# Optimization experiments

Measured on AMD Instinct MI355X. Metric: run time of the kernel, lower is better.

The kernel has to match this reference:

```python
import jax, jax.numpy as jnp
import numpy as np

N_NODES = 50000
N_EDGES = 800000
IN_C, HID_C, OUT_C = 96, 64, 40
ALPHA = 0.2
K = 2
NEG_SLOPE = 0.01  # F.leaky_relu default


def setup_inputs() -> dict:
    key = jax.random.key(0)
    k_x, k_e, k_w0, k_b0, k_w4, k_b4 = jax.random.split(key, 6)
    x = jax.random.normal(k_x, (N_NODES, IN_C), dtype=jnp.float32)
    edge_index = jax.random.randint(k_e, (2, N_EDGES), 0, N_NODES, dtype=jnp.int64)
    # SGConv linear layers (torch.nn.Linear layout: [out, in])
    W0 = jax.random.normal(k_w0, (HID_C, IN_C), dtype=jnp.float32) / np.sqrt(IN_C)
    b0 = jax.random.normal(k_b0, (HID_C,), dtype=jnp.float32) * 0.01
    W4 = jax.random.normal(k_w4, (OUT_C, HID_C), dtype=jnp.float32) / np.sqrt(HID_C)
    b4 = jax.random.normal(k_b4, (OUT_C,), dtype=jnp.float32) * 0.01
    return {"x": x, "edge_index": edge_index, "W0": W0, "b0": b0, "W4": W4, "b4": b4}


def reference(x, edge_index, W0, b0, W4, b4):
    # GCN normalization with self-loops (shared by SGConv and APPNP in PyG):
    # A_hat = A + I, prop(h) = D^{-1/2} A_hat D^{-1/2} h
    n = x.shape[0]
    loops = jnp.arange(n, dtype=edge_index.dtype)
    src = jnp.concatenate([edge_index[0], loops])
    dst = jnp.concatenate([edge_index[1], loops])
    deg = jax.ops.segment_sum(jnp.ones_like(dst, dtype=x.dtype), dst, num_segments=n)
    dinv = jnp.where(deg > 0, jax.lax.rsqrt(deg), 0.0)
    norm = dinv[src] * dinv[dst]  # [E + N]

    def prop(h):
        # gather -> scale -> scatter-add  (irregular memory-bound core op)
        return jax.ops.segment_sum(norm[:, None] * h[src], dst, num_segments=n)

    def sg_prop(h):  # SGConv: K propagation steps, then linear
        for _ in range(K):
            h = prop(h)
        return h

    def appnp(h0):  # APPNP: z_{k+1} = (1-alpha) * prop(z_k) + alpha * h0
        z = h0
        for _ in range(K):
            z = (1.0 - ALPHA) * prop(z) + ALPHA * h0
        return z

    h = sg_prop(x) @ W0.T + b0          # conv0 (SGConv)
    # dropout is identity in eval mode (training=False)
    h = jax.nn.leaky_relu(appnp(h), NEG_SLOPE)   # conv1
    h = jax.nn.leaky_relu(appnp(h), NEG_SLOPE)   # conv2
    h = jax.nn.leaky_relu(appnp(h), NEG_SLOPE)   # conv3
    h = sg_prop(h) @ W4.T + b4          # conv4 (SGConv)
    return jax.nn.log_softmax(h, axis=1)
```

## Files before the change

### kernel.cpp

```cpp
#include <hip/hip_runtime.h>
#include <hip/hip_fp16.h>
#include <math.h>

#define N_NODES 50000
#define N_EDGES 800000
#define IN_C 96
#define HID_C 64
#define OUT_C 40
#define ALPHA 0.2f
#define NEG_SLOPE 0.01f
#define QCAP 131072

typedef _Float16 f16x8 __attribute__((ext_vector_type(8)));
typedef float f32x4 __attribute__((ext_vector_type(4)));

__device__ __forceinline__ int edge_at(const void* ei, int is64, long long pos) {
    return is64 ? (int)((const long long*)ei)[pos] : ((const int*)ei)[pos];
}

__global__ void zero_detect_k(int* deg, int n, int* qtail, const unsigned int* ei, int* flag,
                              __half* bufA, __half* bufB, __half* bufC) {
    int i = blockIdx.x * blockDim.x + threadIdx.x;
    if (i < n) deg[i] = 0;
    if (i < 8) qtail[i] = 0;
    if (i >= 8 && i < 32) {
        int j = i - 8;
        __half* b = (j < 8) ? bufA : (j < 16) ? bufB : bufC;
        ((float4*)b)[(size_t)N_NODES * 8 + (j & 7)] = make_float4(0.f, 0.f, 0.f, 0.f);
    }
    if (i == 0) {
        int is64 = 1;
        for (int j = 1; j < 16; j += 2)
            if (ei[j] != 0u) is64 = 0;
        *flag = is64;
    }
}

__global__ void bucketA_k(const void* ei, const int* flag, int* __restrict__ deg,
                          int* __restrict__ qtail, int2* __restrict__ queue, int E) {
    __shared__ int cnt[8], qb[8];
    int f = *flag;
    int e0 = blockIdx.x * 1024;
    if (threadIdx.x < 8) cnt[threadIdx.x] = 0;
    __syncthreads();
    int s[4], d[4], p[4], r[4];
    #pragma unroll
    for (int k = 0; k < 4; ++k) {
        int e = e0 + threadIdx.x + k * 256;
        if (e < E) {
            d[k] = edge_at(ei, f, (long long)E + e);
            s[k] = edge_at(ei, f, e);
            atomicAdd(&deg[d[k]], 1);
            p[k] = d[k] / (N_NODES / 8);
            if (p[k] > 7) p[k] = 7;
            r[k] = atomicAdd(&cnt[p[k]], 1);
        } else p[k] = -1;
    }
    __syncthreads();
    if (threadIdx.x < 8) qb[threadIdx.x] = atomicAdd(&qtail[threadIdx.x], cnt[threadIdx.x]);
    __syncthreads();
    #pragma unroll
    for (int k = 0; k < 4; ++k) {
        if (p[k] >= 0) {
            int pos = qb[p[k]] + r[k];
            if (pos < QCAP) queue[(size_t)p[k] * QCAP + pos] = make_int2(s[k], d[k]);
        }
    }
}

__global__ void bucketB_k(const int* __restrict__ qtail, const int2* __restrict__ queue,
                          int* __restrict__ cursor, int* __restrict__ csrc) {
    int p = blockIdx.x & 7;
    int j = blockIdx.x >> 3;
    int J = gridDim.x >> 3;
    int n = qtail[p]; if (n > QCAP) n = QCAP;
    const int2* q = queue + (size_t)p * QCAP;
    for (int i = j * blockDim.x + threadIdx.x; i < n; i += J * blockDim.x) {
        int2 e = q[i];
        int pos = atomicAdd(&cursor[e.y], 1);
        csrc[pos] = e.x;
    }
}

__global__ void scan_p1_k(const int* __restrict__ deg, int* __restrict__ part, int n) {
    __shared__ int sm[256];
    int t = threadIdx.x, i = blockIdx.x * 256 + t;
    int v = (i < n) ? ((deg[i] + 3) & ~3) : 0;
    sm[t] = v;
    __syncthreads();
    for (int off = 1; off < 256; off <<= 1) {
        int u = (t >= off) ? sm[t - off] : 0;
        __syncthreads();
        sm[t] += u;
        __syncthreads();
    }
    if (t == 255) part[blockIdx.x] = sm[255];
}

__global__ void scan_p2_k(int* part, int nb, int* rowptr, int n) {
    __shared__ int sm[256];
    int t = threadIdx.x;
    int v = (t < nb) ? part[t] : 0;
    sm[t] = v;
    __syncthreads();
    for (int off = 1; off < 256; off <<= 1) {
        int u = (t >= off) ? sm[t - off] : 0;
        __syncthreads();
        sm[t] += u;
        __syncthreads();
    }
    if (t < nb) part[t] = sm[t] - v;
    if (t == 255) rowptr[n] = sm[255];
}

__global__ void scan_p3_k(const int* __restrict__ deg, const int* __restrict__ part,
                          int* __restrict__ rowptr, int* __restrict__ cursor,
                          float* __restrict__ dinv, int* __restrict__ bcnt,
                          int* __restrict__ csrc, int n) {
    __shared__ int sm[256];
    __shared__ int h[64];
    int t = threadIdx.x, i = blockIdx.x * 256 + t;
    if (t < 64) h[t] = 0;
    int d = (i < n) ? deg[i] : 0;
    int v = (d + 3) & ~3;
    sm[t] = v;
    __syncthreads();
    for (int off = 1; off < 256; off <<= 1) {
        int u = (t >= off) ? sm[t - off] : 0;
        __syncthreads();
        sm[t] += u;
        __syncthreads();
    }
    if (i < n) {
        int excl = sm[t] - v + part[blockIdx.x];
        rowptr[i] = excl;
        cursor[i] = excl;
        dinv[i] = rsqrtf((float)d + 1.0f);
        for (int k = d; k < v; ++k) csrc[excl + k] = N_NODES;
        int dd = d; if (dd > 63) dd = 63;
        atomicAdd(&h[63 - dd], 1);
    }
    __syncthreads();
    if (t < 64) bcnt[blockIdx.x * 64 + t] = h[t];
}

__global__ void bscanA_k(const int* __restrict__ bcnt, int* __restrict__ bbase,
                         int* __restrict__ tot, int nb) {
    __shared__ int sm[256];
    int b = blockIdx.x;
    int t = threadIdx.x;
    int v = (t < nb) ? bcnt[t * 64 + b] : 0;
    sm[t] = v;
    __syncthreads();
    for (int off = 1; off < 256; off <<= 1) {
        int u = (t >= off) ? sm[t - off] : 0;
        __syncthreads();
        sm[t] += u;
        __syncthreads();
    }
    if (t < nb) bbase[t * 64 + b] = sm[t] - v;
    if (t == 255) tot[b] = sm[255];
}

__global__ void perm_k(const int* __restrict__ deg, const int* __restrict__ bbase,
                       const int* __restrict__ tot, int* __restrict__ perm, int n) {
    __shared__ int h[64], bs[64];
    int t = threadIdx.x, i = blockIdx.x * 256 + t;
    if (t < 64) { h[t] = 0; bs[t] = tot[t]; }
    __syncthreads();
    if (t == 0) {
        int run = 0;
        for (int k = 0; k < 64; ++k) { int v = bs[k]; bs[k] = run; run += v; }
    }
    __syncthreads();
    if (i < n) {
        int d = deg[i]; if (d > 63) d = 63;
        int b = 63 - d;
        int rank = atomicAdd(&h[b], 1);
        perm[bs[b] + bbase[blockIdx.x * 64 + b] + rank] = i;
    }
}

__device__ __forceinline__ void add8(float* acc, float4 v) {
    const __half2* hp = (const __half2*)&v;
    #pragma unroll
    for (int j = 0; j < 4; ++j) {
        float2 f = __half22float2(hp[j]);
        acc[2 * j] += f.x;
        acc[2 * j + 1] += f.y;
    }
}

__device__ __forceinline__ void unpack8(float* acc, float4 r) {
    const __half2* hp = (const __half2*)&r;
    #pragma unroll
    for (int j = 0; j < 4; ++j) {
        float2 f = __half22float2(hp[j]);
        acc[2 * j] = f.x;
        acc[2 * j + 1] = f.y;
    }
}

__device__ __forceinline__ void gather4(const float4* __restrict__ in8, int ci,
        const int* __restrict__ csrc, int r0, int r1, float* acc) {
    if (r0 >= r1) return;
    int4 s = *(const int4*)(csrc + r0);
    int i = r0;
    for (; i + 4 < r1; i += 4) {
        float4 v0 = in8[(size_t)s.x * 8 + ci];
        float4 v1 = in8[(size_t)s.y * 8 + ci];
        float4 v2 = in8[(size_t)s.z * 8 + ci];
        float4 v3 = in8[(size_t)s.w * 8 + ci];
        s = *(const int4*)(csrc + i + 4);
        add8(acc, v0); add8(acc, v1); add8(acc, v2); add8(acc, v3);
    }
    {
        float4 v0 = in8[(size_t)s.x * 8 + ci];
        float4 v1 = in8[(size_t)s.y * 8 + ci];
        float4 v2 = in8[(size_t)s.z * 8 + ci];
        float4 v3 = in8[(size_t)s.w * 8 + ci];
        add8(acc, v0); add8(acc, v1); add8(acc, v2); add8(acc, v3);
    }
}

template <bool COMBINE, bool LEAKY, bool BIAS>
__global__ void __launch_bounds__(256) prop64_k(
        const int* __restrict__ perm,
        const int* __restrict__ rowptr, const int* __restrict__ csrc,
        const float* __restrict__ dinv,
        const __half* __restrict__ in, const __half* __restrict__ h0,
        const float* __restrict__ bias,
        __half* __restrict__ out, int N) {
    int g = blockIdx.x * (blockDim.x >> 3) + (threadIdx.x >> 3);
    int ci = threadIdx.x & 7;
    if (g >= N) return;
    int node = perm[g];
    const float4* in8 = (const float4*)in;
    float acc[8];
    unpack8(acc, in8[(size_t)node * 8 + ci]);
    int r0 = rowptr[node], r1 = rowptr[node + 1];
    gather4(in8, ci, csrc, r0, r1, acc);
    float di = dinv[node];
    float sc = di * di;
    float v[8];
    #pragma unroll
    for (int j = 0; j < 8; ++j) v[j] = sc * acc[j];
    if (BIAS) {
        float4 b0v = ((const float4*)bias)[2 * ci];
        float4 b1v = ((const float4*)bias)[2 * ci + 1];
        v[0] += di * b0v.x; v[1] += di * b0v.y; v[2] += di * b0v.z; v[3] += di * b0v.w;
        v[4] += di * b1v.x; v[5] += di * b1v.y; v[6] += di * b1v.z; v[7] += di * b1v.w;
    }
    if (COMBINE) {
        float h[8];
        unpack8(h, ((const float4*)h0)[(size_t)node * 8 + ci]);
        #pragma unroll
        for (int j = 0; j < 8; ++j) v[j] = (1.0f - ALPHA) * v[j] + ALPHA * h[j];
    }
    if (LEAKY) {
        #pragma unroll
        for (int j = 0; j < 8; ++j) v[j] = v[j] > 0.0f ? v[j] : NEG_SLOPE * v[j];
    }
    float4 o;
    __half2* op = (__half2*)&o;
    #pragma unroll
    for (int j = 0; j < 4; ++j)
        op[j] = __float22half2_rn(make_float2(v[2 * j], v[2 * j + 1]));
    ((float4*)out)[(size_t)node * 8 + ci] = o;
}

__global__ void __launch_bounds__(256) prop40_k(
        const int* __restrict__ perm,
        const int* __restrict__ rowptr, const int* __restrict__ csrc,
        const float* __restrict__ dinv,
        const __half* __restrict__ in, __half* __restrict__ out, int N) {
    int g = blockIdx.x * (blockDim.x >> 3) + (threadIdx.x >> 3);
    int ci = threadIdx.x & 7;
    if (g >= N) return;
    int node = perm[g];
    bool act = ci < 5;
    int cc = act ? ci : 0;
    const float4* in4 = (const float4*)in;
    float acc[8];
    unpack8(acc, in4[(size_t)node * 8 + cc]);
    int r0 = rowptr[node], r1 = rowptr[node + 1];
    gather4(in4, cc, csrc, r0, r1, acc);
    if (act) {
        float di = dinv[node];
        float sc = di * di;
        float4 o;
        __half2* op = (__half2*)&o;
        #pragma unroll
        for (int j = 0; j < 4; ++j)
            op[j] = __float22half2_rn(make_float2(sc * acc[2 * j], sc * acc[2 * j + 1]));
        ((float4*)out)[(size_t)node * 8 + ci] = o;
    }
}

__global__ void __launch_bounds__(256) prop40_softmax_k(
        const int* __restrict__ perm,
        const int* __restrict__ rowptr, const int* __restrict__ csrc,
        const float* __restrict__ dinv,
        const __half* __restrict__ in, const float* __restrict__ bias,
        float* __restrict__ out, int N) {
    int g = blockIdx.x * (blockDim.x >> 3) + (threadIdx.x >> 3);
    int ci = threadIdx.x & 7;
    if (g >= N) return;
    int node = perm[g];
    bool act = ci < 5;
    int cc = act ? ci : 0;
    const float4* in4 = (const float4*)in;
    float acc[8];
    unpack8(acc, in4[(size_t)node * 8 + cc]);
    int r0 = rowptr[node], r1 = rowptr[node + 1];
    gather4(in4, cc, csrc, r0, r1, acc);
    float di = dinv[node];
    float v[8];
    if (act) {
        float4 b0v = ((const float4*)bias)[2 * ci];
        float4 b1v = ((const float4*)bias)[2 * ci + 1];
        v[0] = di * acc[0] + b0v.x; v[1] = di * acc[1] + b0v.y;
        v[2] = di * acc[2] + b0v.z; v[3] = di * acc[3] + b0v.w;
        v[4] = di * acc[4] + b1v.x; v[5] = di * acc[5] + b1v.y;
        v[6] = di * acc[6] + b1v.z; v[7] = di * acc[7] + b1v.w;
    } else {
        #pragma unroll
        for (int j = 0; j < 8; ++j) v[j] = -INFINITY;
    }
    float m = v[0];
    #pragma unroll
    for (int j = 1; j < 8; ++j) m = fmaxf(m, v[j]);
    #pragma unroll
    for (int off = 4; off >= 1; off >>= 1) m = fmaxf(m, __shfl_xor(m, off));
    float e = 0.0f;
    if (act) {
        #pragma unroll
        for (int j = 0; j < 8; ++j) e += expf(v[j] - m);
    }
    #pragma unroll
    for (int off = 4; off >= 1; off >>= 1) e += __shfl_xor(e, off);
    float ls = m + logf(e);
    if (act) {
        float4 o0 = make_float4(v[0] - ls, v[1] - ls, v[2] - ls, v[3] - ls);
        float4 o1 = make_float4(v[4] - ls, v[5] - ls, v[6] - ls, v[7] - ls);
        ((float4*)out)[(size_t)node * 10 + 2 * ci] = o0;
        ((float4*)out)[(size_t)node * 10 + 2 * ci + 1] = o1;
    }
}

template <int O, int K, int OP, bool FP32IN, bool SCALE>
__global__ void __launch_bounds__(256) mfma_lin_k(const void* __restrict__ in_,
                                                  const float* __restrict__ W,
                                                  const float* __restrict__ dinv,
                                                  __half* __restrict__ out, int Mtiles) {
    constexpr int P2 = 52;
    __shared__ __half2 wsh[O * P2];
    for (int idx = threadIdx.x; idx < O * (K / 2); idx += 256) {
        int o = idx / (K / 2), kk = idx - o * (K / 2);
        float2 w2 = ((const float2*)W)[o * (K / 2) + kk];
        wsh[o * P2 + kk] = __floats2half2_rn(w2.x, w2.y);
    }
    __syncthreads();
    int wave = (blockIdx.x * 256 + threadIdx.x) >> 6;
    if (wave >= Mtiles) return;
    int lane = threadIdx.x & 63;
    int lm = lane & 15, q = lane >> 4;
    long long m0 = (long long)wave * 16;
    constexpr int NT = (O + 15) / 16;
    f32x4 acc[NT];
    #pragma unroll
    for (int j = 0; j < NT; ++j) acc[j] = (f32x4){0.f, 0.f, 0.f, 0.f};
    const __half* wsp = (const __half*)wsh;
    #pragma unroll
    for (int k0 = 0; k0 < K; k0 += 32) {
        f16x8 a;
        if (FP32IN) {
            const float* xr = (const float*)in_ + (m0 + lm) * K + k0 + q * 8;
            float4 x0 = ((const float4*)xr)[0];
            float4 x1 = ((const float4*)xr)[1];
            a = (f16x8){(_Float16)x0.x, (_Float16)x0.y, (_Float16)x0.z, (_Float16)x0.w,
                        (_Float16)x1.x, (_Float16)x1.y, (_Float16)x1.z, (_Float16)x1.w};
        } else {
            const __half* xr = (const __half*)in_ + (m0 + lm) * K + k0 + q * 8;
            a = *(const f16x8*)xr;
        }
        #pragma unroll
        for (int j = 0; j < NT; ++j) {
            f16x8 b = *(const f16x8*)(wsp + (16 * j + lm) * (2 * P2) + k0 + q * 8);
            acc[j] = __builtin_amdgcn_mfma_f32_16x16x32_f16(a, b, acc[j], 0, 0, 0);
        }
    }
    #pragma unroll
    for (int r = 0; r < 4; ++r) {
        long long m = m0 + q * 4 + r;
        float sc = SCALE ? dinv[m] : 1.0f;
        #pragma unroll
        for (int j = 0; j < NT; ++j) {
            int col = 16 * j + lm;
            if (col < O) out[m * OP + col] = __float2half(acc[j][r] * sc);
        }
    }
}

static inline int cdiv(long long a, long long b) { return (int)((a + b - 1) / b); }
static inline size_t align256(size_t x) { return (x + 255) & ~(size_t)255; }

extern "C" void kernel_launch(void* const* d_in, const int* in_sizes, int n_in,
                              void* d_out, int out_size, void* d_ws, size_t ws_size,
                              hipStream_t stream) {
    const float* x  = (const float*)d_in[0];
    const void*  ei = d_in[1];
    const float* W0 = (const float*)d_in[2];
    const float* b0 = (const float*)d_in[3];
    const float* W4 = (const float*)d_in[4];
    const float* b4 = (const float*)d_in[5];
    float* out = (float*)d_out;

    const int N = N_NODES, E = N_EDGES;
    const int NB = cdiv(N, 256);
    const int EP = E + 4 * N;
    char* ws = (char*)d_ws;
    int*    flag   = (int*)ws;     ws += 256;
    int*    deg    = (int*)ws;     ws += align256((size_t)N * 4);
    int*    rowptr = (int*)ws;     ws += align256((size_t)(N + 1) * 4);
    int*    cursor = (int*)ws;     ws += align256((size_t)N * 4);
    int*    part   = (int*)ws;     ws += align256(256 * 4);
    int*    bcnt   = (int*)ws;     ws += align256((size_t)NB * 64 * 4);
    int*    bbase  = (int*)ws;     ws += align256((size_t)NB * 64 * 4);
    int*    tot    = (int*)ws;     ws += align256(64 * 4);
    int*    qtail  = (int*)ws;     ws += align256(8 * 4);
    int*    perm   = (int*)ws;     ws += align256((size_t)N * 4);
    float*  dinv   = (float*)ws;   ws += align256((size_t)N * 4);
    int*    csrc   = (int*)ws;     ws += align256((size_t)EP * 4);
    int2*   queue  = (int2*)ws;    ws += align256((size_t)8 * QCAP * 8);
    __half* bufA   = (__half*)ws;  ws += align256((size_t)(N + 1) * HID_C * 2);
    __half* bufB   = (__half*)ws;  ws += align256((size_t)(N + 1) * HID_C * 2);
    __half* bufC   = (__half*)ws;  ws += align256((size_t)(N + 1) * HID_C * 2);

    const int T = 256;
    const int MT = N / 16;
    const int LB = cdiv(MT, 4);
    const int P64B = cdiv(N, T / 8);

    zero_detect_k<<<cdiv(N, T), T, 0, stream>>>(deg, N, qtail, (const unsigned int*)ei, flag,
                                                bufA, bufB, bufC);
    bucketA_k<<<cdiv(E, 1024), T, 0, stream>>>(ei, flag, deg, qtail, queue, E);
    scan_p1_k<<<NB, 256, 0, stream>>>(deg, part, N);
    scan_p2_k<<<1, 256, 0, stream>>>(part, NB, rowptr, N);
    scan_p3_k<<<NB, 256, 0, stream>>>(deg, part, rowptr, cursor, dinv, bcnt, csrc, N);
    bscanA_k<<<64, 256, 0, stream>>>(bcnt, bbase, tot, NB);
    perm_k<<<NB, 256, 0, stream>>>(deg, bbase, tot, perm, N);
    bucketB_k<<<8 * 64, T, 0, stream>>>(qtail, queue, cursor, csrc);

    mfma_lin_k<HID_C, IN_C, HID_C, true, true><<<LB, 256, 0, stream>>>(x, W0, dinv, bufA, MT);
    prop64_k<false, false, false><<<P64B, T, 0, stream>>>(
        perm, rowptr, csrc, dinv, bufA, nullptr, nullptr, bufB, N);
    prop64_k<false, false, true><<<P64B, T, 0, stream>>>(
        perm, rowptr, csrc, dinv, bufB, nullptr, b0, bufC, N);

    for (int r = 0; r < 3; ++r) {
        prop64_k<true, false, false><<<P64B, T, 0, stream>>>(
            perm, rowptr, csrc, dinv, bufC, bufC, nullptr, bufB, N);
        prop64_k<true, true, false><<<P64B, T, 0, stream>>>(
            perm, rowptr, csrc, dinv, bufB, bufC, nullptr, bufC, N);
    }

    mfma_lin_k<OUT_C, HID_C, HID_C, false, false><<<LB, 256, 0, stream>>>(
        bufC, W4, dinv, bufA, MT);
    prop40_k<<<P64B, T, 0, stream>>>(perm, rowptr, csrc, dinv, bufA, bufB, N);
    prop40_softmax_k<<<P64B, T, 0, stream>>>(perm, rowptr, csrc, dinv, bufB, b4, out, N);
}
```

Baseline: 316.5 us.

## Merge scan phases and perm/bucketB kernels, add nontemporal loads for streamed data

Folds the two-pass block scan into one kernel, using a last-block-done atomic counter so the final block scans the partial sums, and fuses the perm and bucketB kernels into one launch that splits its blocks between the two roles. This removes two kernel launches and the gaps between them in the preprocessing chain. Edge indices, queue entries and CSR source reads now use nontemporal loads so streamed data is less likely to evict the gathered features from cache. The risks are the threadfence/atomic overhead in the merged scan and that NBLK is hardcoded to the node count.

```diff
diff --git a/kernel.cpp b/kernel.cpp
--- a/kernel.cpp
+++ b/kernel.cpp
@@ -10,12 +10,16 @@
 #define ALPHA 0.2f
 #define NEG_SLOPE 0.01f
 #define QCAP 131072
+#define NBLK 196
 
 typedef _Float16 f16x8 __attribute__((ext_vector_type(8)));
 typedef float f32x4 __attribute__((ext_vector_type(4)));
+typedef int i32x4 __attribute__((ext_vector_type(4)));
+typedef int i32x2 __attribute__((ext_vector_type(2)));
 
 __device__ __forceinline__ int edge_at(const void* ei, int is64, long long pos) {
-    return is64 ? (int)((const long long*)ei)[pos] : ((const int*)ei)[pos];
+    return is64 ? (int)__builtin_nontemporal_load((const long long*)ei + pos)
+                : __builtin_nontemporal_load((const int*)ei + pos);
 }
 
 __global__ void zero_detect_k(int* deg, int n, int* qtail, const unsigned int* ei, int* flag,
@@ -23,6 +27,7 @@
     int i = blockIdx.x * blockDim.x + threadIdx.x;
     if (i < n) deg[i] = 0;
     if (i < 8) qtail[i] = 0;
+    if (i == 1) flag[1] = 0;
     if (i >= 8 && i < 32) {
         int j = i - 8;
         __half* b = (j < 8) ? bufA : (j < 16) ? bufB : bufC;
@@ -68,22 +73,10 @@
     }
 }
 
-__global__ void bucketB_k(const int* __restrict__ qtail, const int2* __restrict__ queue,
-                          int* __restrict__ cursor, int* __restrict__ csrc) {
-    int p = blockIdx.x & 7;
-    int j = blockIdx.x >> 3;
-    int J = gridDim.x >> 3;
-    int n = qtail[p]; if (n > QCAP) n = QCAP;
-    const int2* q = queue + (size_t)p * QCAP;
-    for (int i = j * blockDim.x + threadIdx.x; i < n; i += J * blockDim.x) {
-        int2 e = q[i];
-        int pos = atomicAdd(&cursor[e.y], 1);
-        csrc[pos] = e.x;
-    }
-}
-
-__global__ void scan_p1_k(const int* __restrict__ deg, int* __restrict__ part, int n) {
+__global__ void scan_p12_k(const int* __restrict__ deg, int* __restrict__ part,
+                           int* __restrict__ rowptr, int* __restrict__ done, int n) {
     __shared__ int sm[256];
+    __shared__ int lastFlag;
     int t = threadIdx.x, i = blockIdx.x * 256 + t;
     int v = (i < n) ? ((deg[i] + 3) & ~3) : 0;
     sm[t] = v;
@@ -95,13 +88,12 @@
         __syncthreads();
     }
     if (t == 255) part[blockIdx.x] = sm[255];
-}
-
-__global__ void scan_p2_k(int* part, int nb, int* rowptr, int n) {
-    __shared__ int sm[256];
-    int t = threadIdx.x;
-    int v = (t < nb) ? part[t] : 0;
-    sm[t] = v;
+    __threadfence();
+    if (t == 0) lastFlag = (atomicAdd(done, 1) == (int)gridDim.x - 1);
+    __syncthreads();
+    if (!lastFlag) return;
+    int pv = (t < NBLK) ? part[t] : 0;
+    sm[t] = pv;
     __syncthreads();
     for (int off = 1; off < 256; off <<= 1) {
         int u = (t >= off) ? sm[t - off] : 0;
@@ -109,7 +101,7 @@
         sm[t] += u;
         __syncthreads();
     }
-    if (t < nb) part[t] = sm[t] - v;
+    if (t < NBLK) part[t] = sm[t] - pv;
     if (t == 255) rowptr[n] = sm[255];
 }
 
@@ -162,22 +154,39 @@
     if (t == 255) tot[b] = sm[255];
 }
 
-__global__ void perm_k(const int* __restrict__ deg, const int* __restrict__ bbase,
-                       const int* __restrict__ tot, int* __restrict__ perm, int n) {
-    __shared__ int h[64], bs[64];
-    int t = threadIdx.x, i = blockIdx.x * 256 + t;
-    if (t < 64) { h[t] = 0; bs[t] = tot[t]; }
-    __syncthreads();
-    if (t == 0) {
-        int run = 0;
-        for (int k = 0; k < 64; ++k) { int v = bs[k]; bs[k] = run; run += v; }
-    }
-    __syncthreads();
-    if (i < n) {
-        int d = deg[i]; if (d > 63) d = 63;
-        int b = 63 - d;
-        int rank = atomicAdd(&h[b], 1);
-        perm[bs[b] + bbase[blockIdx.x * 64 + b] + rank] = i;
+__global__ void perm_bucketB_k(const int* __restrict__ deg, const int* __restrict__ bbase,
+                               const int* __restrict__ tot, int* __restrict__ perm,
+                               const int* __restrict__ qtail, const int2* __restrict__ queue,
+                               int* __restrict__ cursor, int* __restrict__ csrc, int n) {
+    int t = threadIdx.x;
+    if (blockIdx.x < NBLK) {
+        __shared__ int h[64], bs[64];
+        int i = blockIdx.x * 256 + t;
+        if (t < 64) { h[t] = 0; bs[t] = tot[t]; }
+        __syncthreads();
+        if (t == 0) {
+            int run = 0;
+            for (int k = 0; k < 64; ++k) { int v = bs[k]; bs[k] = run; run += v; }
+        }
+        __syncthreads();
+        if (i < n) {
+            int d = deg[i]; if (d > 63) d = 63;
+            int b = 63 - d;
+            int rank = atomicAdd(&h[b], 1);
+            perm[bs[b] + bbase[blockIdx.x * 64 + b] + rank] = i;
+        }
+    } else {
+        int vb = blockIdx.x - NBLK;
+        int J = (gridDim.x - NBLK) >> 3;
+        int p = vb & 7;
+        int j = vb >> 3;
+        int nq = qtail[p]; if (nq > QCAP) nq = QCAP;
+        const int2* q = queue + (size_t)p * QCAP;
+        for (int i2 = j * 256 + t; i2 < nq; i2 += J * 256) {
+            i32x2 e = __builtin_nontemporal_load((const i32x2*)q + i2);
+            int pos = atomicAdd(&cursor[e[1]], 1);
+            csrc[pos] = e[0];
+        }
     }
 }
 
@@ -204,21 +213,21 @@
 __device__ __forceinline__ void gather4(const float4* __restrict__ in8, int ci,
         const int* __restrict__ csrc, int r0, int r1, float* acc) {
     if (r0 >= r1) return;
-    int4 s = *(const int4*)(csrc + r0);
+    i32x4 s = __builtin_nontemporal_load((const i32x4*)(csrc + r0));
     int i = r0;
     for (; i + 4 < r1; i += 4) {
-        float4 v0 = in8[(size_t)s.x * 8 + ci];
-        float4 v1 = in8[(size_t)s.y * 8 + ci];
-        float4 v2 = in8[(size_t)s.z * 8 + ci];
-        float4 v3 = in8[(size_t)s.w * 8 + ci];
-        s = *(const int4*)(csrc + i + 4);
+        float4 v0 = in8[(size_t)s[0] * 8 + ci];
+        float4 v1 = in8[(size_t)s[1] * 8 + ci];
+        float4 v2 = in8[(size_t)s[2] * 8 + ci];
+        float4 v3 = in8[(size_t)s[3] * 8 + ci];
+        s = __builtin_nontemporal_load((const i32x4*)(csrc + i + 4));
         add8(acc, v0); add8(acc, v1); add8(acc, v2); add8(acc, v3);
     }
     {
-        float4 v0 = in8[(size_t)s.x * 8 + ci];
-        float4 v1 = in8[(size_t)s.y * 8 + ci];
-        float4 v2 = in8[(size_t)s.z * 8 + ci];
-        float4 v3 = in8[(size_t)s.w * 8 + ci];
+        float4 v0 = in8[(size_t)s[0] * 8 + ci];
+        float4 v1 = in8[(size_t)s[1] * 8 + ci];
+        float4 v2 = in8[(size_t)s[2] * 8 + ci];
+        float4 v3 = in8[(size_t)s[3] * 8 + ci];
         add8(acc, v0); add8(acc, v1); add8(acc, v2); add8(acc, v3);
     }
 }
@@ -417,7 +426,6 @@
     float* out = (float*)d_out;
 
     const int N = N_NODES, E = N_EDGES;
-    const int NB = cdiv(N, 256);
     const int EP = E + 4 * N;
     char* ws = (char*)d_ws;
     int*    flag   = (int*)ws;     ws += 256;
@@ -425,8 +433,8 @@
     int*    rowptr = (int*)ws;     ws += align256((size_t)(N + 1) * 4);
     int*    cursor = (int*)ws;     ws += align256((size_t)N * 4);
     int*    part   = (int*)ws;     ws += align256(256 * 4);
-    int*    bcnt   = (int*)ws;     ws += align256((size_t)NB * 64 * 4);
-    int*    bbase  = (int*)ws;     ws += align256((size_t)NB * 64 * 4);
+    int*    bcnt   = (int*)ws;     ws += align256((size_t)NBLK * 64 * 4);
+    int*    bbase  = (int*)ws;     ws += align256((size_t)NBLK * 64 * 4);
     int*    tot    = (int*)ws;     ws += align256(64 * 4);
     int*    qtail  = (int*)ws;     ws += align256(8 * 4);
     int*    perm   = (int*)ws;     ws += align256((size_t)N * 4);
@@ -445,12 +453,11 @@
     zero_detect_k<<<cdiv(N, T), T, 0, stream>>>(deg, N, qtail, (const unsigned int*)ei, flag,
                                                 bufA, bufB, bufC);
     bucketA_k<<<cdiv(E, 1024), T, 0, stream>>>(ei, flag, deg, qtail, queue, E);
-    scan_p1_k<<<NB, 256, 0, stream>>>(deg, part, N);
-    scan_p2_k<<<1, 256, 0, stream>>>(part, NB, rowptr, N);
-    scan_p3_k<<<NB, 256, 0, stream>>>(deg, part, rowptr, cursor, dinv, bcnt, csrc, N);
-    bscanA_k<<<64, 256, 0, stream>>>(bcnt, bbase, tot, NB);
-    perm_k<<<NB, 256, 0, stream>>>(deg, bbase, tot, perm, N);
-    bucketB_k<<<8 * 64, T, 0, stream>>>(qtail, queue, cursor, csrc);
+    scan_p12_k<<<NBLK, 256, 0, stream>>>(deg, part, rowptr, flag + 1, N);
+    scan_p3_k<<<NBLK, 256, 0, stream>>>(deg, part, rowptr, cursor, dinv, bcnt, csrc, N);
+    bscanA_k<<<64, 256, 0, stream>>>(bcnt, bbase, tot, NBLK);
+    perm_bucketB_k<<<NBLK + 512, T, 0, stream>>>(deg, bbase, tot, perm,
+                                                 qtail, queue, cursor, csrc, N);
 
     mfma_lin_k<HID_C, IN_C, HID_C, true, true><<<LB, 256, 0, stream>>>(x, W0, dinv, bufA, MT);
     prop64_k<false, false, false><<<P64B, T, 0, stream>>>(
```

Result: slower. 353.3 us (+11.6%).
